# Optimization experiments

Measured on AMD Instinct MI355X. Metric: run time of the kernel, lower is better.

Reference implementation:

```python
import jax, jax.numpy as jnp
import numpy as np
from jax import lax

EPS = 1e-5
DN = ('NCHW', 'OIHW', 'NCHW')


def ternarize(w):
    # Standard TWN-style ternarization: {-1, 0, +1} with threshold 0.7*mean|w|
    thr = 0.7 * jnp.mean(jnp.abs(w))
    return jnp.sign(w) * (jnp.abs(w) > thr).astype(w.dtype)


def conv(x, w, b=None):
    y = lax.conv_general_dilated(x, w, (1, 1), 'VALID', dimension_numbers=DN)
    if b is not None:
        y = y + b[None, :, None, None]
    return y


def bn(x, g, be, m, v):
    inv = g / jnp.sqrt(v + EPS)
    return x * inv[None, :, None, None] + (be - m * inv)[None, :, None, None]


def maxpool2(x):
    return lax.reduce_window(x, -jnp.inf, lax.max, (1, 1, 2, 2), (1, 1, 2, 2), 'VALID')


def setup_inputs() -> dict:
    key = jax.random.key(0)
    ks = jax.random.split(key, 21)
    d = {}
    d['x'] = jax.random.normal(ks[0], (8192, 1, 28, 28), jnp.float32)
    d['w1'] = ternarize(jax.random.normal(ks[1], (32, 1, 5, 5), jnp.float32))
    d['b1'] = jax.random.normal(ks[2], (32,), jnp.float32) * 0.1
    d['g1'] = jax.random.uniform(ks[3], (32,), jnp.float32, 0.5, 1.5)
    d['be1'] = jax.random.normal(ks[4], (32,), jnp.float32) * 0.1
    d['m1'] = jax.random.normal(ks[5], (32,), jnp.float32) * 0.1
    d['v1'] = jax.random.uniform(ks[6], (32,), jnp.float32, 0.5, 1.5)
    d['w2'] = ternarize(jax.random.normal(ks[7], (64, 32, 5, 5), jnp.float32))
    d['b2'] = jax.random.normal(ks[8], (64,), jnp.float32) * 0.1
    d['g2'] = jax.random.uniform(ks[9], (64,), jnp.float32, 0.5, 1.5)
    d['be2'] = jax.random.normal(ks[10], (64,), jnp.float32) * 0.1
    d['m2'] = jax.random.normal(ks[11], (64,), jnp.float32) * 0.1
    d['v2'] = jax.random.uniform(ks[12], (64,), jnp.float32, 0.5, 1.5)
    d['w3'] = ternarize(jax.random.normal(ks[13], (512, 1024, 1, 1), jnp.float32))
    d['b3'] = jax.random.normal(ks[14], (512,), jnp.float32) * 0.1
    d['g3'] = jax.random.uniform(ks[15], (512,), jnp.float32, 0.5, 1.5)
    d['be3'] = jax.random.normal(ks[16], (512,), jnp.float32) * 0.1
    d['m3'] = jax.random.normal(ks[17], (512,), jnp.float32) * 0.1
    d['v3'] = jax.random.uniform(ks[18], (512,), jnp.float32, 0.5, 1.5)
    d['w4'] = jax.random.normal(ks[19], (10, 512, 1, 1), jnp.float32) * 0.05
    return d


def reference(x, w1, b1, g1, be1, m1, v1, w2, b2, g2, be2, m2, v2,
              w3, b3, g3, be3, m3, v3, w4):
    h = conv(x, w1, b1)                       # [B,32,24,24]
    h = maxpool2(jax.nn.relu(bn(h, g1, be1, m1, v1)))   # [B,32,12,12]
    h = conv(h, w2, b2)                       # [B,64,8,8]
    h = maxpool2(jax.nn.relu(bn(h, g2, be2, m2, v2)))   # [B,64,4,4]
    h = h.reshape(-1, 1024, 1, 1)             # flatten C,H,W
    h = jax.nn.relu(bn(conv(h, w3, b3), g3, be3, m3, v3))  # [B,512,1,1]
    h = conv(h, w4)                            # [B,10,1,1]
    return h.reshape(-1, 10)
```

## Files before the change

### kernel.cpp

```cpp
#include <hip/hip_runtime.h>

#define EPS 1e-5f

typedef float f32x4 __attribute__((ext_vector_type(4)));
typedef short short8_t __attribute__((ext_vector_type(8)));
typedef unsigned int uint4v __attribute__((ext_vector_type(4)));
typedef unsigned short ushort_t;

__global__ void prep_kernel(const float* __restrict__ b1, const float* __restrict__ g1,
                            const float* __restrict__ be1, const float* __restrict__ m1,
                            const float* __restrict__ v1,
                            const float* __restrict__ b2, const float* __restrict__ g2,
                            const float* __restrict__ be2, const float* __restrict__ m2,
                            const float* __restrict__ v2,
                            const float* __restrict__ b3, const float* __restrict__ g3,
                            const float* __restrict__ be3, const float* __restrict__ m3,
                            const float* __restrict__ v3,
                            const float* __restrict__ w1, const float* __restrict__ w2,
                            const float* __restrict__ w3,
                            ushort_t* __restrict__ w1frag, ushort_t* __restrict__ w2frag,
                            ushort_t* __restrict__ w3frag, float* __restrict__ prm) {
  int tid = blockIdx.x * blockDim.x + threadIdx.x;
  int stride = gridDim.x * blockDim.x;
  for (int c = tid; c < 32; c += stride) {
    float s = g1[c] / sqrtf(v1[c] + EPS);
    prm[c] = s;
    prm[32 + c] = (b1[c] - m1[c]) * s + be1[c];
  }
  for (int c = tid; c < 64; c += stride) {
    float s = g2[c] / sqrtf(v2[c] + EPS);
    prm[64 + c] = s;
    prm[128 + c] = (b2[c] - m2[c]) * s + be2[c];
  }
  for (int c = tid; c < 512; c += stride) {
    float s = g3[c] / sqrtf(v3[c] + EPS);
    prm[192 + c] = s;
    prm[704 + c] = (b3[c] - m3[c]) * s + be3[c];
  }
  for (int i = tid; i < 2 * 2 * 64 * 8; i += stride) {
    const int j = i & 7;
    const int l = (i >> 3) & 63;
    const int nt = (i >> 9) & 1;
    const int p = i >> 10;
    const int oc = nt * 16 + (l & 15);
    const int t = (l >> 4) * 8 + j;
    const float v = (t < 25) ? w1[oc * 25 + t] : 0.f;
    const unsigned u = __float_as_uint(v);
    const ushort_t hi = (ushort_t)(u >> 16);
    const float r = v - __uint_as_float(u & 0xffff0000u);
    const ushort_t lo = (ushort_t)(__float_as_uint(r) >> 16);
    w1frag[i] = p ? lo : hi;
  }
  for (int i = tid; i < 25 * 4 * 64 * 8; i += stride) {
    const int kk = i >> 11;
    const int r = i & 2047;
    const int nt = r >> 9;
    const int r2 = r & 511;
    const int l = r2 >> 3;
    const int j = r2 & 7;
    const int oc = nt * 16 + (l & 15);
    const int ic = (l >> 4) * 8 + j;
    w2frag[i] = (ushort_t)(__float_as_uint(w2[oc * 800 + ic * 25 + kk]) >> 16);
  }
  for (int i = tid; i < 32 * 32 * 64 * 8; i += stride) {
    const int ks = i >> 14;
    const int r = i & 16383;
    const int ntg = r >> 9;
    const int r2 = r & 511;
    const int l = r2 >> 3;
    const int j = r2 & 7;
    const int oc = ntg * 16 + (l & 15);
    const int k = ks * 32 + (l >> 4) * 8 + j;
    w3frag[i] = (ushort_t)(__float_as_uint(w3[oc * 1024 + k]) >> 16);
  }
}

__launch_bounds__(128)
__global__ void conv12_kernel(const float* __restrict__ x,
                              const ushort_t* __restrict__ w1frag,
                              const ushort_t* __restrict__ w2frag,
                              const float* __restrict__ prm,
                              ushort_t* __restrict__ h2pH, ushort_t* __restrict__ h2pL) {
  __shared__ __align__(16) unsigned char lds[26240];

  const int tid = threadIdx.x;
  const int w = tid >> 6, l = tid & 63;
  const int b = blockIdx.x;
  const int m15 = l & 15, g = l >> 4;

  float* imgf = (float*)lds;
  ushort_t* insA = (ushort_t*)(lds + 3200);

  const float* xb = x + (size_t)b * 784;
  for (int i = tid; i < 196; i += 128) ((float4*)imgf)[i] = ((const float4*)xb)[i];
  if (tid < 16) imgf[784 + tid] = 0.f;

  short8_t B1h[2], B1l[2];
#pragma unroll
  for (int nt = 0; nt < 2; ++nt) {
    B1h[nt] = *(const short8_t*)(w1frag + (size_t)(nt * 64 + l) * 8);
    B1l[nt] = *(const short8_t*)(w1frag + (size_t)((2 + nt) * 64 + l) * 8);
  }

  int off[8];
#pragma unroll
  for (int j = 0; j < 8; ++j) {
    const int t = g * 8 + j;
    const int ky = t / 5, kx = t - ky * 5;
    off[j] = (t < 25) ? (ky * 28 + kx) : 0;
  }

  float s1[2], sh1[2], s2[4], sh2[4];
#pragma unroll
  for (int nt = 0; nt < 2; ++nt) {
    s1[nt] = prm[nt * 16 + m15];
    sh1[nt] = prm[32 + nt * 16 + m15];
  }
#pragma unroll
  for (int nt = 0; nt < 4; ++nt) {
    s2[nt] = prm[64 + nt * 16 + m15];
    sh2[nt] = prm[128 + nt * 16 + m15];
  }
  __syncthreads();

#pragma unroll 1
  for (int i = 0; i < 18; ++i) {
    const int mt = w * 18 + i;
    const int q = mt * 16 + m15;
    const int p_pool = q >> 2, sub = q & 3;
    const int py = p_pool / 12, px = p_pool - py * 12;
    const int Y = 2 * py + (sub >> 1), X = 2 * px + (sub & 1);
    const float* pixb = imgf + Y * 28 + X;
    float v[8];
#pragma unroll
    for (int j = 0; j < 8; ++j) v[j] = pixb[off[j]];
    uint4v hv, lv;
#pragma unroll
    for (int k = 0; k < 4; ++k) {
      const unsigned u0 = __float_as_uint(v[2 * k]);
      const unsigned u1 = __float_as_uint(v[2 * k + 1]);
      hv[k] = (u0 >> 16) | (u1 & 0xffff0000u);
      const float r0 = v[2 * k] - __uint_as_float(u0 & 0xffff0000u);
      const float r1 = v[2 * k + 1] - __uint_as_float(u1 & 0xffff0000u);
      lv[k] = (__float_as_uint(r0) >> 16) | (__float_as_uint(r1) & 0xffff0000u);
    }
    const short8_t ah = __builtin_bit_cast(short8_t, hv);
    const short8_t al = __builtin_bit_cast(short8_t, lv);

    f32x4 c0 = {0.f, 0.f, 0.f, 0.f}, c1 = {0.f, 0.f, 0.f, 0.f};
    c0 = __builtin_amdgcn_mfma_f32_16x16x32_bf16(ah, B1h[0], c0, 0, 0, 0);
    c1 = __builtin_amdgcn_mfma_f32_16x16x32_bf16(ah, B1h[1], c1, 0, 0, 0);
    c0 = __builtin_amdgcn_mfma_f32_16x16x32_bf16(al, B1h[0], c0, 0, 0, 0);
    c1 = __builtin_amdgcn_mfma_f32_16x16x32_bf16(al, B1h[1], c1, 0, 0, 0);
    c0 = __builtin_amdgcn_mfma_f32_16x16x32_bf16(ah, B1l[0], c0, 0, 0, 0);
    c1 = __builtin_amdgcn_mfma_f32_16x16x32_bf16(ah, B1l[1], c1, 0, 0, 0);

    const int cell = mt * 4 + g;
#pragma unroll
    for (int nt = 0; nt < 2; ++nt) {
      const f32x4 c = nt ? c1 : c0;
      const float pv = fmaxf(fmaxf(c[0], c[1]), fmaxf(c[2], c[3]));
      const float a = fmaxf(fmaf(pv, s1[nt], sh1[nt]), 0.f);
      const unsigned u = __float_as_uint(a);
      const float r = a - __uint_as_float(u & 0xffff0000u);
      const int ic = nt * 16 + m15;
      insA[cell * 40 + ic] = (ushort_t)(u >> 16);
      insA[5760 + cell * 40 + ic] = (ushort_t)(__float_as_uint(r) >> 16);
    }
  }
  __syncthreads();

  const int sy = (m15 & 3) >> 1, sx = m15 & 1;
  const int X2 = 2 * (m15 >> 2) + sx;

  f32x4 acc[2][4];
#pragma unroll
  for (int m = 0; m < 2; ++m)
#pragma unroll
    for (int nt = 0; nt < 4; ++nt) acc[m][nt] = (f32x4){0.f, 0.f, 0.f, 0.f};

#pragma unroll 1
  for (int pass = 0; pass < 5; ++pass) {
    short8_t wr[5][4];
#pragma unroll
    for (int kx = 0; kx < 5; ++kx)
#pragma unroll
      for (int nt = 0; nt < 4; ++nt)
        wr[kx][nt] = *(const short8_t*)(w2frag + (size_t)(((pass * 5 + kx) * 4 + nt) * 64 + l) * 8);
#pragma unroll
    for (int kx = 0; kx < 5; ++kx) {
#pragma unroll
      for (int m = 0; m < 2; ++m) {
        const int mt2 = 2 * w + m;
        const int cellin = (2 * mt2 + sy + pass) * 12 + X2 + kx;
        const short8_t aH = *(const short8_t*)(insA + cellin * 40 + g * 8);
        const short8_t aL = *(const short8_t*)(insA + 5760 + cellin * 40 + g * 8);
#pragma unroll
        for (int nt = 0; nt < 4; ++nt) {
          acc[m][nt] = __builtin_amdgcn_mfma_f32_16x16x32_bf16(aH, wr[kx][nt], acc[m][nt], 0, 0, 0);
          acc[m][nt] = __builtin_amdgcn_mfma_f32_16x16x32_bf16(aL, wr[kx][nt], acc[m][nt], 0, 0, 0);
        }
      }
    }
  }

  const size_t ob = (size_t)b * 1024;
#pragma unroll
  for (int m = 0; m < 2; ++m) {
    const int cell2 = (2 * w + m) * 4 + g;
#pragma unroll
    for (int nt = 0; nt < 4; ++nt) {
      const f32x4 c = acc[m][nt];
      const float pv = fmaxf(fmaxf(c[0], c[1]), fmaxf(c[2], c[3]));
      const float a = fmaxf(fmaf(pv, s2[nt], sh2[nt]), 0.f);
      const unsigned u = __float_as_uint(a);
      const float r = a - __uint_as_float(u & 0xffff0000u);
      const int oc = nt * 16 + m15;
      h2pH[ob + oc * 16 + cell2] = (ushort_t)(u >> 16);
      h2pL[ob + oc * 16 + cell2] = (ushort_t)(__float_as_uint(r) >> 16);
    }
  }
}

__launch_bounds__(256)
__global__ void fc3_kernel(const ushort_t* __restrict__ h2pH, const ushort_t* __restrict__ h2pL,
                           const ushort_t* __restrict__ w3frag, const float* __restrict__ prm,
                           float* __restrict__ a3) {
  const int orig = blockIdx.x + (blockIdx.y << 3);
  const int xcd = orig & 7;
  const int j = orig >> 3;
  const int ytile = (xcd << 4) | (j >> 3);
  const int xtile = j & 7;
  const int n0 = xtile * 64;
  const int m0 = ytile * 64;
  const int w = threadIdx.x >> 6, l = threadIdx.x & 63;
  const int mrow = m0 + w * 16 + (l & 15);
  const int kc8 = (l >> 4) * 8;

  const ushort_t* aHp = h2pH + (size_t)mrow * 1024 + kc8;
  const ushort_t* aLp = h2pL + (size_t)mrow * 1024 + kc8;
  const ushort_t* bp = w3frag + (size_t)(n0 >> 4) * 512 + (size_t)l * 8;

  f32x4 accH[4], accL[4];
#pragma unroll
  for (int t = 0; t < 4; ++t) {
    accH[t] = (f32x4){0.f, 0.f, 0.f, 0.f};
    accL[t] = (f32x4){0.f, 0.f, 0.f, 0.f};
  }

#pragma unroll 2
  for (int ks = 0; ks < 32; ++ks) {
    const short8_t aH = *(const short8_t*)(aHp + ks * 32);
    const short8_t aL = *(const short8_t*)(aLp + ks * 32);
    const ushort_t* bks = bp + (size_t)ks * 16384;
#pragma unroll
    for (int t = 0; t < 4; ++t) {
      const short8_t bb = *(const short8_t*)(bks + t * 512);
      accH[t] = __builtin_amdgcn_mfma_f32_16x16x32_bf16(aH, bb, accH[t], 0, 0, 0);
      accL[t] = __builtin_amdgcn_mfma_f32_16x16x32_bf16(aL, bb, accL[t], 0, 0, 0);
    }
  }

#pragma unroll
  for (int t = 0; t < 4; ++t) {
    const int oc = n0 + t * 16 + (l & 15);
    const float s = prm[192 + oc], sh = prm[704 + oc];
#pragma unroll
    for (int r = 0; r < 4; ++r) {
      const int m = m0 + w * 16 + (l >> 4) * 4 + r;
      a3[(size_t)m * 512 + oc] = fmaxf(fmaf(accH[t][r] + accL[t][r], s, sh), 0.f);
    }
  }
}

__launch_bounds__(256)
__global__ void fc4_kernel(const float* __restrict__ a3, const float* __restrict__ w4,
                           float* __restrict__ out, int B) {
  const int w = threadIdx.x >> 6, l = threadIdx.x & 63;
  const int b = blockIdx.x * 4 + w;
  if (b >= B) return;
  const float4* ar = (const float4*)(a3 + (size_t)b * 512);
  const float4 a0 = ar[l * 2];
  const float4 a1 = ar[l * 2 + 1];
#pragma unroll
  for (int j = 0; j < 10; ++j) {
    const float4* wr = (const float4*)(w4 + j * 512);
    const float4 w0 = wr[l * 2];
    const float4 w1 = wr[l * 2 + 1];
    float sv = a0.x * w0.x + a0.y * w0.y + a0.z * w0.z + a0.w * w0.w +
               a1.x * w1.x + a1.y * w1.y + a1.z * w1.z + a1.w * w1.w;
#pragma unroll
    for (int off = 1; off < 64; off <<= 1) sv += __shfl_xor(sv, off);
    if (l == 0) out[(size_t)b * 10 + j] = sv;
  }
}

extern "C" void kernel_launch(void* const* d_in, const int* in_sizes, int n_in,
                              void* d_out, int out_size, void* d_ws, size_t ws_size,
                              hipStream_t stream) {
  const float* x  = (const float*)d_in[0];
  const float* w1 = (const float*)d_in[1];
  const float* b1 = (const float*)d_in[2];
  const float* g1 = (const float*)d_in[3];
  const float* be1 = (const float*)d_in[4];
  const float* m1 = (const float*)d_in[5];
  const float* v1 = (const float*)d_in[6];
  const float* w2 = (const float*)d_in[7];
  const float* b2 = (const float*)d_in[8];
  const float* g2 = (const float*)d_in[9];
  const float* be2 = (const float*)d_in[10];
  const float* m2 = (const float*)d_in[11];
  const float* v2 = (const float*)d_in[12];
  const float* w3 = (const float*)d_in[13];
  const float* b3 = (const float*)d_in[14];
  const float* g3 = (const float*)d_in[15];
  const float* be3 = (const float*)d_in[16];
  const float* m3 = (const float*)d_in[17];
  const float* v3 = (const float*)d_in[18];
  const float* w4 = (const float*)d_in[19];

  const int B = in_sizes[0] / 784;

  float* prm = (float*)d_ws;
  ushort_t* w1frag = (ushort_t*)(prm + 1216);
  ushort_t* w2frag = w1frag + 2048;
  ushort_t* w3frag = w2frag + 51200;
  ushort_t* h2pH = w3frag + 524288;
  ushort_t* h2pL = h2pH + (size_t)B * 1024;
  float* a3 = (float*)(h2pL + (size_t)B * 1024);

  prep_kernel<<<64, 256, 0, stream>>>(b1, g1, be1, m1, v1, b2, g2, be2, m2, v2,
                                      b3, g3, be3, m3, v3, w1, w2, w3,
                                      w1frag, w2frag, w3frag, prm);
  conv12_kernel<<<B, 128, 0, stream>>>(x, w1frag, w2frag, prm, h2pH, h2pL);
  dim3 g3d(8, B / 64);
  fc3_kernel<<<g3d, 256, 0, stream>>>(h2pH, h2pL, w3frag, prm, a3);
  fc4_kernel<<<(B + 3) / 4, 256, 0, stream>>>(a3, w4, (float*)d_out, B);
}
```

Before: 283.1 us.

## Double conv12 block to 256 threads and precompute split-bf16 image once

conv12 now runs 4 waves per block, so each wave does half the conv1 tiles and a single conv2 m-tile, with launch bounds set for higher occupancy. The input image is stored once in LDS as packed hi/lo bf16 pairs, which removes the per-tap float splitting arithmetic from the conv1 loop. conv2 now loads activations per ky row and streams weight fragments per kx, instead of holding a large 5x4 weight register array. fc3 merges the hi and lo accumulators into one and unrolls the loop further, which lengthens the MFMA dependency chains in exchange for fewer registers.

```diff
diff --git a/kernel.cpp b/kernel.cpp
--- a/kernel.cpp
+++ b/kernel.cpp
@@ -75,7 +75,7 @@
   }
 }
 
-__launch_bounds__(128)
+__launch_bounds__(256, 5)
 __global__ void conv12_kernel(const float* __restrict__ x,
                               const ushort_t* __restrict__ w1frag,
                               const ushort_t* __restrict__ w2frag,
@@ -88,12 +88,17 @@
   const int b = blockIdx.x;
   const int m15 = l & 15, g = l >> 4;
 
-  float* imgf = (float*)lds;
+  unsigned* imgP = (unsigned*)lds;
   ushort_t* insA = (ushort_t*)(lds + 3200);
 
   const float* xb = x + (size_t)b * 784;
-  for (int i = tid; i < 196; i += 128) ((float4*)imgf)[i] = ((const float4*)xb)[i];
-  if (tid < 16) imgf[784 + tid] = 0.f;
+  for (int i = tid; i < 784; i += 256) {
+    const float v = xb[i];
+    const unsigned u = __float_as_uint(v);
+    const float r = v - __uint_as_float(u & 0xffff0000u);
+    imgP[i] = (u & 0xffff0000u) | (__float_as_uint(r) >> 16);
+  }
+  if (tid < 16) imgP[784 + tid] = 0u;
 
   short8_t B1h[2], B1l[2];
 #pragma unroll
@@ -123,26 +128,22 @@
   }
   __syncthreads();
 
-#pragma unroll 1
-  for (int i = 0; i < 18; ++i) {
-    const int mt = w * 18 + i;
+#pragma unroll 3
+  for (int i = 0; i < 9; ++i) {
+    const int mt = w * 9 + i;
     const int q = mt * 16 + m15;
     const int p_pool = q >> 2, sub = q & 3;
     const int py = p_pool / 12, px = p_pool - py * 12;
     const int Y = 2 * py + (sub >> 1), X = 2 * px + (sub & 1);
-    const float* pixb = imgf + Y * 28 + X;
-    float v[8];
-#pragma unroll
-    for (int j = 0; j < 8; ++j) v[j] = pixb[off[j]];
+    const unsigned* pixb = imgP + Y * 28 + X;
+    unsigned pv[8];
+#pragma unroll
+    for (int j = 0; j < 8; ++j) pv[j] = pixb[off[j]];
     uint4v hv, lv;
 #pragma unroll
     for (int k = 0; k < 4; ++k) {
-      const unsigned u0 = __float_as_uint(v[2 * k]);
-      const unsigned u1 = __float_as_uint(v[2 * k + 1]);
-      hv[k] = (u0 >> 16) | (u1 & 0xffff0000u);
-      const float r0 = v[2 * k] - __uint_as_float(u0 & 0xffff0000u);
-      const float r1 = v[2 * k + 1] - __uint_as_float(u1 & 0xffff0000u);
-      lv[k] = (__float_as_uint(r0) >> 16) | (__float_as_uint(r1) & 0xffff0000u);
+      hv[k] = (pv[2 * k] >> 16) | (pv[2 * k + 1] & 0xffff0000u);
+      lv[k] = (pv[2 * k] & 0xffffu) | (pv[2 * k + 1] << 16);
     }
     const short8_t ah = __builtin_bit_cast(short8_t, hv);
     const short8_t al = __builtin_bit_cast(short8_t, lv);
@@ -159,8 +160,8 @@
 #pragma unroll
     for (int nt = 0; nt < 2; ++nt) {
       const f32x4 c = nt ? c1 : c0;
-      const float pv = fmaxf(fmaxf(c[0], c[1]), fmaxf(c[2], c[3]));
-      const float a = fmaxf(fmaf(pv, s1[nt], sh1[nt]), 0.f);
+      const float pvv = fmaxf(fmaxf(c[0], c[1]), fmaxf(c[2], c[3]));
+      const float a = fmaxf(fmaf(pvv, s1[nt], sh1[nt]), 0.f);
       const unsigned u = __float_as_uint(a);
       const float r = a - __uint_as_float(u & 0xffff0000u);
       const int ic = nt * 16 + m15;
@@ -173,52 +174,49 @@
   const int sy = (m15 & 3) >> 1, sx = m15 & 1;
   const int X2 = 2 * (m15 >> 2) + sx;
 
-  f32x4 acc[2][4];
-#pragma unroll
-  for (int m = 0; m < 2; ++m)
-#pragma unroll
-    for (int nt = 0; nt < 4; ++nt) acc[m][nt] = (f32x4){0.f, 0.f, 0.f, 0.f};
+  f32x4 acc[4];
+#pragma unroll
+  for (int nt = 0; nt < 4; ++nt) acc[nt] = (f32x4){0.f, 0.f, 0.f, 0.f};
 
 #pragma unroll 1
-  for (int pass = 0; pass < 5; ++pass) {
-    short8_t wr[5][4];
-#pragma unroll
-    for (int kx = 0; kx < 5; ++kx)
-#pragma unroll
-      for (int nt = 0; nt < 4; ++nt)
-        wr[kx][nt] = *(const short8_t*)(w2frag + (size_t)(((pass * 5 + kx) * 4 + nt) * 64 + l) * 8);
+  for (int ky = 0; ky < 5; ++ky) {
+    const int rowb = (2 * w + sy + ky) * 12 + X2;
+    short8_t a[5][2];
 #pragma unroll
     for (int kx = 0; kx < 5; ++kx) {
-#pragma unroll
-      for (int m = 0; m < 2; ++m) {
-        const int mt2 = 2 * w + m;
-        const int cellin = (2 * mt2 + sy + pass) * 12 + X2 + kx;
-        const short8_t aH = *(const short8_t*)(insA + cellin * 40 + g * 8);
-        const short8_t aL = *(const short8_t*)(insA + 5760 + cellin * 40 + g * 8);
-#pragma unroll
-        for (int nt = 0; nt < 4; ++nt) {
-          acc[m][nt] = __builtin_amdgcn_mfma_f32_16x16x32_bf16(aH, wr[kx][nt], acc[m][nt], 0, 0, 0);
-          acc[m][nt] = __builtin_amdgcn_mfma_f32_16x16x32_bf16(aL, wr[kx][nt], acc[m][nt], 0, 0, 0);
-        }
-      }
+      a[kx][0] = *(const short8_t*)(insA + (rowb + kx) * 40 + g * 8);
+      a[kx][1] = *(const short8_t*)(insA + 5760 + (rowb + kx) * 40 + g * 8);
+    }
+#pragma unroll
+    for (int kx = 0; kx < 5; ++kx) {
+      const ushort_t* wp = w2frag + (size_t)(((ky * 5 + kx) * 4) * 64 + l) * 8;
+      const short8_t b0 = *(const short8_t*)(wp);
+      const short8_t b1 = *(const short8_t*)(wp + 512);
+      const short8_t b2 = *(const short8_t*)(wp + 1024);
+      const short8_t b3 = *(const short8_t*)(wp + 1536);
+      acc[0] = __builtin_amdgcn_mfma_f32_16x16x32_bf16(a[kx][0], b0, acc[0], 0, 0, 0);
+      acc[0] = __builtin_amdgcn_mfma_f32_16x16x32_bf16(a[kx][1], b0, acc[0], 0, 0, 0);
+      acc[1] = __builtin_amdgcn_mfma_f32_16x16x32_bf16(a[kx][0], b1, acc[1], 0, 0, 0);
+      acc[1] = __builtin_amdgcn_mfma_f32_16x16x32_bf16(a[kx][1], b1, acc[1], 0, 0, 0);
+      acc[2] = __builtin_amdgcn_mfma_f32_16x16x32_bf16(a[kx][0], b2, acc[2], 0, 0, 0);
+      acc[2] = __builtin_amdgcn_mfma_f32_16x16x32_bf16(a[kx][1], b2, acc[2], 0, 0, 0);
+      acc[3] = __builtin_amdgcn_mfma_f32_16x16x32_bf16(a[kx][0], b3, acc[3], 0, 0, 0);
+      acc[3] = __builtin_amdgcn_mfma_f32_16x16x32_bf16(a[kx][1], b3, acc[3], 0, 0, 0);
     }
   }
 
   const size_t ob = (size_t)b * 1024;
-#pragma unroll
-  for (int m = 0; m < 2; ++m) {
-    const int cell2 = (2 * w + m) * 4 + g;
-#pragma unroll
-    for (int nt = 0; nt < 4; ++nt) {
-      const f32x4 c = acc[m][nt];
-      const float pv = fmaxf(fmaxf(c[0], c[1]), fmaxf(c[2], c[3]));
-      const float a = fmaxf(fmaf(pv, s2[nt], sh2[nt]), 0.f);
-      const unsigned u = __float_as_uint(a);
-      const float r = a - __uint_as_float(u & 0xffff0000u);
-      const int oc = nt * 16 + m15;
-      h2pH[ob + oc * 16 + cell2] = (ushort_t)(u >> 16);
-      h2pL[ob + oc * 16 + cell2] = (ushort_t)(__float_as_uint(r) >> 16);
-    }
+  const int cell2 = w * 4 + g;
+#pragma unroll
+  for (int nt = 0; nt < 4; ++nt) {
+    const f32x4 c = acc[nt];
+    const float pvv = fmaxf(fmaxf(c[0], c[1]), fmaxf(c[2], c[3]));
+    const float a = fmaxf(fmaf(pvv, s2[nt], sh2[nt]), 0.f);
+    const unsigned u = __float_as_uint(a);
+    const float r = a - __uint_as_float(u & 0xffff0000u);
+    const int oc = nt * 16 + m15;
+    h2pH[ob + oc * 16 + cell2] = (ushort_t)(u >> 16);
+    h2pL[ob + oc * 16 + cell2] = (ushort_t)(__float_as_uint(r) >> 16);
   }
 }
 
@@ -241,14 +239,11 @@
   const ushort_t* aLp = h2pL + (size_t)mrow * 1024 + kc8;
   const ushort_t* bp = w3frag + (size_t)(n0 >> 4) * 512 + (size_t)l * 8;
 
-  f32x4 accH[4], accL[4];
-#pragma unroll
-  for (int t = 0; t < 4; ++t) {
-    accH[t] = (f32x4){0.f, 0.f, 0.f, 0.f};
-    accL[t] = (f32x4){0.f, 0.f, 0.f, 0.f};
-  }
-
-#pragma unroll 2
+  f32x4 acc[4];
+#pragma unroll
+  for (int t = 0; t < 4; ++t) acc[t] = (f32x4){0.f, 0.f, 0.f, 0.f};
+
+#pragma unroll 4
   for (int ks = 0; ks < 32; ++ks) {
     const short8_t aH = *(const short8_t*)(aHp + ks * 32);
     const short8_t aL = *(const short8_t*)(aLp + ks * 32);
@@ -256,8 +251,8 @@
 #pragma unroll
     for (int t = 0; t < 4; ++t) {
       const short8_t bb = *(const short8_t*)(bks + t * 512);
-      accH[t] = __builtin_amdgcn_mfma_f32_16x16x32_bf16(aH, bb, accH[t], 0, 0, 0);
-      accL[t] = __builtin_amdgcn_mfma_f32_16x16x32_bf16(aL, bb, accL[t], 0, 0, 0);
+      acc[t] = __builtin_amdgcn_mfma_f32_16x16x32_bf16(aH, bb, acc[t], 0, 0, 0);
+      acc[t] = __builtin_amdgcn_mfma_f32_16x16x32_bf16(aL, bb, acc[t], 0, 0, 0);
     }
   }
 
@@ -268,7 +263,7 @@
 #pragma unroll
     for (int r = 0; r < 4; ++r) {
       const int m = m0 + w * 16 + (l >> 4) * 4 + r;
-      a3[(size_t)m * 512 + oc] = fmaxf(fmaf(accH[t][r] + accL[t][r], s, sh), 0.f);
+      a3[(size_t)m * 512 + oc] = fmaxf(fmaf(acc[t][r], s, sh), 0.f);
     }
   }
 }
@@ -332,7 +327,7 @@
   prep_kernel<<<64, 256, 0, stream>>>(b1, g1, be1, m1, v1, b2, g2, be2, m2, v2,
                                       b3, g3, be3, m3, v3, w1, w2, w3,
                                       w1frag, w2frag, w3frag, prm);
-  conv12_kernel<<<B, 128, 0, stream>>>(x, w1frag, w2frag, prm, h2pH, h2pL);
+  conv12_kernel<<<B, 256, 0, stream>>>(x, w1frag, w2frag, prm, h2pH, h2pL);
   dim3 g3d(8, B / 64);
   fc3_kernel<<<g3d, 256, 0, stream>>>(h2pH, h2pL, w3frag, prm, a3);
   fc4_kernel<<<(B + 3) / 4, 256, 0, stream>>>(a3, w4, (float*)d_out, B);
```

Measured after the change: 299.1 us. +5.6%, slower.
